# Kernel optimization log

Measured on AMD Instinct MI355X. Metric: run time of the kernel, lower is better.

## Reference

```python
import jax, jax.numpy as jnp
import numpy as np

B, QT, KT = 4, 1024, 1024
Q_SIZE, K_SIZE, EMB, HEADS = 1024, 1024, 1024, 8
HEAD_DIM = EMB // HEADS


def setup_inputs() -> dict:
    key = jax.random.key(0)
    ks = jax.random.split(key, 8)
    query = jax.random.normal(ks[0], (B, QT, Q_SIZE), dtype=jnp.float32)
    key_t = jax.random.normal(ks[1], (B, KT, K_SIZE), dtype=jnp.float32)
    mask = jax.random.randint(ks[2], (B, QT, KT), 0, 2, dtype=jnp.int32)
    # Linear weights stored as (in, out); torch Linear computes x @ W.T, equivalent here.
    sq = 1.0 / np.sqrt(Q_SIZE)
    sk = 1.0 / np.sqrt(K_SIZE)
    se = 1.0 / np.sqrt(EMB)
    Wq = jax.random.uniform(ks[3], (Q_SIZE, EMB), jnp.float32, -sq, sq)
    Wk = jax.random.uniform(ks[4], (K_SIZE, EMB), jnp.float32, -sk, sk)
    Wv = jax.random.uniform(ks[5], (K_SIZE, EMB), jnp.float32, -sk, sk)
    Wu = jax.random.uniform(ks[6], (EMB, EMB), jnp.float32, -se, se)
    bu = jax.random.uniform(ks[7], (EMB,), jnp.float32, -se, se)
    return {"query": query, "key": key_t, "mask": mask,
            "Wq": Wq, "Wk": Wk, "Wv": Wv, "Wu": Wu, "bu": bu}


def reference(query, key, mask, Wq, Wk, Wv, Wu, bu):
    b, q_t, _ = query.shape
    k_t = key.shape[1]
    q = (query @ Wq).reshape(b, q_t, HEADS, HEAD_DIM)   # b i n d
    k = (key @ Wk).reshape(b, k_t, HEADS, HEAD_DIM)     # b j n d
    v = (key @ Wv).reshape(b, k_t, HEADS, HEAD_DIM)
    # NOTE: original module defines self.scale but never applies it.
    att_score = jnp.einsum('bind,bjnd->bijn', q, k)
    att_score = jnp.where(mask[..., None] == 0, jnp.float32(-1e9), att_score)
    att_prob = jax.nn.softmax(att_score, axis=2)        # softmax over key axis j
    att_vec = jnp.einsum('bijn,bjnd->bind', att_prob, v).reshape(b, q_t, EMB)
    return att_vec @ Wu + bu
```

## Files before the change

### kernel.cpp

```cpp
#include <hip/hip_runtime.h>
#include <hip/hip_bf16.h>


typedef __attribute__((ext_vector_type(8))) short bf16x8;
typedef __attribute__((ext_vector_type(4))) float f32x4;

static constexpr int BB = 4;
static constexpr int TT = 1024;
static constexpr int EE = 1024;
static constexpr int HH = 8;
static constexpr int DD = 128;

static __device__ __forceinline__ unsigned short f2b(float x) {
  union { float f; unsigned int u; } c; c.f = x;
  unsigned int r = c.u + 0x7fffu + ((c.u >> 16) & 1u);
  return (unsigned short)(r >> 16);
}

static __device__ __forceinline__ unsigned int cvtpk(float lo, float hi) {
  unsigned int r;
  asm("v_cvt_pk_bf16_f32 %0, %1, %2" : "=v"(r) : "v"(lo), "v"(hi));
  return r;
}

static __device__ __forceinline__ float exp2x(float x) {
  float r;
  asm("v_exp_f32 %0, %1" : "=v"(r) : "v"(x));
  return r;
}

static __device__ __forceinline__ void gload_lds16(const void* g, void* l) {
  __builtin_amdgcn_global_load_lds(
      (const __attribute__((address_space(1))) unsigned int*)g,
      (__attribute__((address_space(3))) unsigned int*)l, 16, 0, 0);
}

__global__ __launch_bounds__(256) void cvt_kernel(
    const float* __restrict__ qf, const float* __restrict__ kf,
    unsigned short* __restrict__ qb, unsigned short* __restrict__ kb) {
  int i = blockIdx.x * 256 + threadIdx.x;
  float4 a = ((const float4*)qf)[i];
  ushort4 oa; oa.x = f2b(a.x); oa.y = f2b(a.y); oa.z = f2b(a.z); oa.w = f2b(a.w);
  ((ushort4*)qb)[i] = oa;
  float4 b = ((const float4*)kf)[i];
  ushort4 ob; ob.x = f2b(b.x); ob.y = f2b(b.y); ob.z = f2b(b.z); ob.w = f2b(b.w);
  ((ushort4*)kb)[i] = ob;
}

struct WT4 { const float* src[4]; unsigned short* dst[4]; float scale[4]; };

__global__ __launch_bounds__(256) void wtrans_kernel(WT4 wt) {
  const float* src = wt.src[blockIdx.z];
  unsigned short* dst = wt.dst[blockIdx.z];
  const float sc = wt.scale[blockIdx.z];
  __shared__ float tile[32][33];
  int n0 = blockIdx.x * 32, k0 = blockIdx.y * 32;
  int tx = threadIdx.x, ty = threadIdx.y;
#pragma unroll
  for (int i = 0; i < 4; ++i)
    tile[ty + i * 8][tx] = src[(size_t)(k0 + ty + i * 8) * EE + n0 + tx];
  __syncthreads();
#pragma unroll
  for (int i = 0; i < 4; ++i)
    dst[(size_t)(n0 + ty + i * 8) * EE + k0 + tx] = f2b(tile[tx][ty + i * 8] * sc);
}

__global__ __launch_bounds__(256) void vtrans_kernel(
    const unsigned short* __restrict__ vp, unsigned short* __restrict__ vt) {
  int bh = blockIdx.z; int b = bh >> 3, h = bh & 7;
  int d0 = blockIdx.x * 32, kt0 = blockIdx.y * 32;
  __shared__ unsigned short tile[32][33];
  int tx = threadIdx.x, ty = threadIdx.y;
#pragma unroll
  for (int i = 0; i < 4; ++i)
    tile[ty + i * 8][tx] =
        vp[(size_t)(b * TT + kt0 + ty + i * 8) * EE + h * DD + d0 + tx];
  __syncthreads();
#pragma unroll
  for (int i = 0; i < 4; ++i)
    vt[(size_t)((b * HH + h) * DD + d0 + ty + i * 8) * TT + kt0 + tx] =
        tile[tx][ty + i * 8];
}

__global__ __launch_bounds__(256) void maskpack_kernel(
    const int* __restrict__ mask, unsigned long long* __restrict__ mbits) {
  int row = blockIdx.x * 4 + (threadIdx.x >> 6);
  int lane = threadIdx.x & 63;
  const int* mrow = mask + (size_t)row * TT;
  unsigned long long myw = 0;
#pragma unroll
  for (int jw = 0; jw < 16; ++jw) {
    unsigned long long bal = __ballot(mrow[jw * 64 + lane] != 0);
    if (lane == jw) myw = bal;
  }
  if (lane < 16) mbits[(size_t)row * 16 + lane] = myw;
}

static __device__ __forceinline__ void gemm_core(
    const unsigned short* __restrict__ A, const unsigned short* __restrict__ Bt,
    unsigned short* __restrict__ Cb) {
  constexpr int K = EE, N = EE;
  __shared__ __align__(16) unsigned short As[128 * 64];
  __shared__ __align__(16) unsigned short Bs[128 * 64];
  const int tid = threadIdx.x, lane = tid & 63, w = tid >> 6;
  const int wm = w >> 1, wn = w & 1;
  const int bm = blockIdx.x, bn = blockIdx.y;
  const int g4 = lane >> 4, l15 = lane & 15;

  f32x4 acc[4][4] = {};

  for (int kt = 0; kt < K / 64; ++kt) {
    const int k0 = kt * 64;
#pragma unroll
    for (int it = 0; it < 4; ++it) {
      int idx = it * 256 + tid;
      int r = idx >> 3, c = (idx & 7) ^ (r & 7);
      gload_lds16(A + (size_t)(bm * 128 + r) * K + k0 + c * 8, As + idx * 8);
      gload_lds16(Bt + (size_t)(bn * 128 + r) * K + k0 + c * 8, Bs + idx * 8);
    }
    __syncthreads();
    bf16x8 af[2][4], bf[2][4];
#pragma unroll
    for (int kc2 = 0; kc2 < 2; ++kc2) {
      int co = ((kc2 * 4 + g4) ^ (l15 & 7)) * 8;
#pragma unroll
      for (int i = 0; i < 4; ++i) {
        af[kc2][i] = *(const bf16x8*)(As + (wm * 64 + i * 16 + l15) * 64 + co);
        bf[kc2][i] = *(const bf16x8*)(Bs + (wn * 64 + i * 16 + l15) * 64 + co);
      }
    }
#pragma unroll
    for (int kc2 = 0; kc2 < 2; ++kc2)
#pragma unroll
      for (int i = 0; i < 4; ++i)
#pragma unroll
        for (int j = 0; j < 4; ++j)
          acc[i][j] = __builtin_amdgcn_mfma_f32_16x16x32_bf16(
              af[kc2][i], bf[kc2][j], acc[i][j], 0, 0, 0);
    __syncthreads();
  }

  const int rr = g4 * 4;
#pragma unroll
  for (int i = 0; i < 4; ++i)
#pragma unroll
    for (int j = 0; j < 4; ++j) {
      int row = bm * 128 + wm * 64 + i * 16 + rr;
      int col = bn * 128 + wn * 64 + j * 16 + l15;
#pragma unroll
      for (int r = 0; r < 4; ++r)
        Cb[(size_t)(row + r) * N + col] = f2b(acc[i][j][r]);
    }
}

struct Gemm3 { const unsigned short* A[3]; const unsigned short* Bt[3];
               unsigned short* C[3]; };

__global__ __launch_bounds__(256) void proj_gemm_kernel(Gemm3 g) {
  int z = blockIdx.z;
  gemm_core(g.A[z], g.Bt[z], g.C[z]);
}

__global__ __launch_bounds__(256) void out_gemm_kernel(
    const unsigned short* __restrict__ A, const unsigned short* __restrict__ Bt,
    float* __restrict__ Cf, const float* __restrict__ bias) {
  constexpr int K = EE, N = EE;
  __shared__ __align__(16) unsigned short As[64 * 32];
  __shared__ __align__(16) unsigned short Bs[128 * 32];
  const int tid = threadIdx.x, lane = tid & 63, w = tid >> 6;
  const int wm = w >> 1, wn = w & 1;
  const int bm = blockIdx.x, bn = blockIdx.y;
  const int g4 = lane >> 4, l15 = lane & 15;

  f32x4 acc[2][4] = {};

  for (int kt = 0; kt < K / 32; ++kt) {
    const int k0 = kt * 32;
    {
      int row = tid >> 2, c = tid & 3;
      gload_lds16(A + (size_t)(bm * 64 + row) * K + k0 + c * 8, As + tid * 8);
    }
#pragma unroll
    for (int it = 0; it < 2; ++it) {
      int idx = it * 256 + tid;
      int row = idx >> 2, c = idx & 3;
      gload_lds16(Bt + (size_t)(bn * 128 + row) * K + k0 + c * 8, Bs + idx * 8);
    }
    __syncthreads();
    bf16x8 af[2], bf[4];
#pragma unroll
    for (int i = 0; i < 2; ++i)
      af[i] = *(const bf16x8*)(As + (wm * 32 + i * 16 + l15) * 32 + g4 * 8);
#pragma unroll
    for (int j = 0; j < 4; ++j)
      bf[j] = *(const bf16x8*)(Bs + (wn * 64 + j * 16 + l15) * 32 + g4 * 8);
#pragma unroll
    for (int i = 0; i < 2; ++i)
#pragma unroll
      for (int j = 0; j < 4; ++j)
        acc[i][j] = __builtin_amdgcn_mfma_f32_16x16x32_bf16(af[i], bf[j],
                                                            acc[i][j], 0, 0, 0);
    __syncthreads();
  }

  const int rr = g4 * 4;
#pragma unroll
  for (int i = 0; i < 2; ++i)
#pragma unroll
    for (int j = 0; j < 4; ++j) {
      int row = bm * 64 + wm * 32 + i * 16 + rr;
      int col = bn * 128 + wn * 64 + j * 16 + l15;
#pragma unroll
      for (int r = 0; r < 4; ++r)
        Cf[(size_t)(row + r) * N + col] = acc[i][j][r] + bias[col];
    }
}

__global__ __launch_bounds__(256) void attn_kernel(
    const unsigned short* __restrict__ q, const unsigned short* __restrict__ k,
    const unsigned short* __restrict__ vt,
    const unsigned long long* __restrict__ mbits,
    unsigned short* __restrict__ av) {
  extern __shared__ __align__(16) char smem[];

  const int tid = threadIdx.x, lane = tid & 63, w = tid >> 6;
  const int orig = blockIdx.x + 16 * blockIdx.y + 128 * blockIdx.z;
  const int qt = (orig >> 3) & 15;
  const int pair = ((orig & 7) << 2) | (orig >> 7);
  const int h = pair & 7, b = pair >> 3;
  const int i0 = qt * 64 + w * 16;
  const int g4 = lane >> 4, l15 = lane & 15;
  const int swz = (l15 & 7) << 4;

  bf16x8 aq[4];
  {
    const unsigned short* qb =
        q + (size_t)(b * TT + i0 + l15) * EE + h * DD + g4 * 8;
#pragma unroll
    for (int kc = 0; kc < 4; ++kc) aq[kc] = *(const bf16x8*)(qb + kc * 32);
  }

  const unsigned short* kb0 = k + (size_t)(b * TT) * EE + h * DD;
  const unsigned short* vb0 = vt + (size_t)((b * HH + h) * DD) * TT;
  const unsigned short* kptr[4];
  const unsigned short* vptr[4];
  int chunkb[4];
#pragma unroll
  for (int p = 0; p < 4; ++p) {
    int base = p * 256 + w * 64;
    int idx = base + lane;
    int kr = idx >> 4, kcc = (idx & 15) ^ (kr & 7);
    kptr[p] = kb0 + (size_t)kr * EE + kcc * 8;
    int vr = idx >> 3, vcc = (idx & 7) ^ (vr & 7);
    vptr[p] = vb0 + (size_t)vr * TT + vcc * 8;
    chunkb[p] = base * 16;
  }

  const unsigned long long* mb = mbits + ((size_t)(b * TT + i0 + l15) << 4);
  unsigned long long mcur = mb[0];

  int kb_[4], vb_[2];
#pragma unroll
  for (int kc = 0; kc < 4; ++kc)
    kb_[kc] = l15 * 256 + ((kc * 64 + g4 * 16) ^ swz);
#pragma unroll
  for (int h2 = 0; h2 < 2; ++h2)
    vb_[h2] = 32768 + l15 * 128 + ((h2 * 64 + g4 * 16) ^ swz);

#pragma unroll
  for (int p = 0; p < 4; ++p) {
    gload_lds16(kptr[p], smem + chunkb[p]);
    gload_lds16(vptr[p], smem + 32768 + chunkb[p]);
  }
#pragma unroll
  for (int p = 0; p < 4; ++p) { kptr[p] += 64 * EE; vptr[p] += 64; }

  f32x4 oacc[8] = {};
  float mrun = -__builtin_inff(), lrun = 0.f;

  __syncthreads();
  int bufoff = 0;

  for (int t = 0; t < 16; ++t) {
    if (t > 0) __builtin_amdgcn_s_barrier();

    unsigned long long mnext = 0;
    if (t < 15) {
      mnext = mb[t + 1];
      int dst = bufoff ^ 16384;
#pragma unroll
      for (int p = 0; p < 4; ++p) {
        gload_lds16(kptr[p], smem + dst + chunkb[p]);
        gload_lds16(vptr[p], smem + 32768 + dst + chunkb[p]);
      }
#pragma unroll
      for (int p = 0; p < 4; ++p) { kptr[p] += 64 * EE; vptr[p] += 64; }
      asm volatile("s_waitcnt vmcnt(8)" ::: "memory");
      __builtin_amdgcn_sched_barrier(0);
    } else {
      asm volatile("s_waitcnt vmcnt(0)" ::: "memory");
      __builtin_amdgcn_sched_barrier(0);
    }

    f32x4 sacc[4] = {};
    __builtin_amdgcn_s_setprio(1);
#pragma unroll
    for (int kc = 0; kc < 4; ++kc)
#pragma unroll
      for (int nt = 0; nt < 4; ++nt) {
        bf16x8 bk = *(const bf16x8*)(smem + kb_[kc] + nt * 4096);
        sacc[nt] = __builtin_amdgcn_mfma_f32_16x16x32_bf16(bk, aq[kc],
                                                           sacc[nt], 0, 0, 0);
      }
    __builtin_amdgcn_s_setprio(0);

    {
      unsigned int wlo = (unsigned int)mcur, whi = (unsigned int)(mcur >> 32);
#pragma unroll
      for (int nt = 0; nt < 4; ++nt) {
        unsigned int ww = (nt < 2) ? wlo : whi;
        int bb = (nt & 1) * 16 + g4 * 4;
#pragma unroll
        for (int r = 0; r < 4; ++r)
          if (((ww >> (bb + r)) & 1u) == 0u) sacc[nt][r] = -1e9f;
      }
    }

    float mx = sacc[0][0];
#pragma unroll
    for (int nt = 0; nt < 4; ++nt)
#pragma unroll
      for (int r = 0; r < 4; ++r) mx = fmaxf(mx, sacc[nt][r]);
    mx = fmaxf(mx, __shfl_xor(mx, 16, 64));
    mx = fmaxf(mx, __shfl_xor(mx, 32, 64));

    if (__any(mx > mrun + 8.f)) {
      float mnew = fmaxf(mrun, mx);
      float sc = exp2x(mrun - mnew);
      lrun *= sc;
      mrun = mnew;
      float scO[4];
#pragma unroll
      for (int r = 0; r < 4; ++r)
        scO[r] = __shfl(sc, (lane & 48) | (((lane & 48) >> 2) + r), 64);
#pragma unroll
      for (int dt = 0; dt < 8; ++dt)
#pragma unroll
        for (int r = 0; r < 4; ++r) oacc[dt][r] *= scO[r];
    }

    float p[4][4];
    float s0 = 0.f;
#pragma unroll
    for (int nt = 0; nt < 4; ++nt)
#pragma unroll
      for (int r = 0; r < 4; ++r) {
        float pv = exp2x(sacc[nt][r] - mrun);
        p[nt][r] = pv;
        s0 += pv;
      }
    s0 += __shfl_xor(s0, 16, 64);
    s0 += __shfl_xor(s0, 32, 64);
    lrun += s0;

    unsigned int paw[2][4];
#pragma unroll
    for (int h2 = 0; h2 < 2; ++h2) {
      unsigned int D0a = cvtpk(p[2 * h2][0], p[2 * h2][1]);
      unsigned int D1a = cvtpk(p[2 * h2][2], p[2 * h2][3]);
      unsigned int D0b = cvtpk(p[2 * h2 + 1][0], p[2 * h2 + 1][1]);
      unsigned int D1b = cvtpk(p[2 * h2 + 1][2], p[2 * h2 + 1][3]);
      unsigned int r1 = __shfl_xor(g4 < 2 ? D0a : D0b, 16, 64);
      unsigned int r2 = __shfl_xor(g4 < 2 ? D1a : D1b, 16, 64);
      unsigned int r3 = __shfl_xor(g4 == 0 ? D0b : D0a, 32, 64);
      unsigned int r4 = __shfl_xor(g4 == 0 ? D1b : D1a, 32, 64);
      unsigned int r5 = __shfl_xor(g4 == 2 ? D0a : D0b, 48, 64);
      unsigned int r6 = __shfl_xor(g4 == 2 ? D1a : D1b, 48, 64);
      paw[h2][0] = g4 == 0 ? D0a : g4 == 1 ? r5 : g4 == 2 ? r3 : r1;
      paw[h2][1] = g4 == 0 ? D1a : g4 == 1 ? r6 : g4 == 2 ? r4 : r2;
      paw[h2][2] = g4 == 0 ? r1 : g4 == 1 ? r3 : g4 == 2 ? r5 : D0b;
      paw[h2][3] = g4 == 0 ? r2 : g4 == 1 ? r4 : g4 == 2 ? r6 : D1b;
    }

    __builtin_amdgcn_s_setprio(1);
#pragma unroll
    for (int h2 = 0; h2 < 2; ++h2) {
      union { unsigned int u[4]; bf16x8 v; } pau;
      pau.u[0] = paw[h2][0]; pau.u[1] = paw[h2][1];
      pau.u[2] = paw[h2][2]; pau.u[3] = paw[h2][3];
#pragma unroll
      for (int dt = 0; dt < 8; ++dt) {
        bf16x8 bv = *(const bf16x8*)(smem + vb_[h2] + dt * 2048);
        oacc[dt] = __builtin_amdgcn_mfma_f32_16x16x32_bf16(pau.v, bv, oacc[dt],
                                                           0, 0, 0);
      }
    }
    __builtin_amdgcn_s_setprio(0);

    bufoff ^= 16384;
#pragma unroll
    for (int kc = 0; kc < 4; ++kc) kb_[kc] ^= 16384;
#pragma unroll
    for (int h2 = 0; h2 < 2; ++h2) vb_[h2] ^= 16384;
    mcur = mnext;
  }

  float linv[4];
#pragma unroll
  for (int r = 0; r < 4; ++r)
    linv[r] = 1.f / __shfl(lrun, (lane & 48) | (((lane & 48) >> 2) + r), 64);
  unsigned short* ob =
      av + (size_t)(b * TT + i0 + g4 * 4) * EE + h * DD + l15;
#pragma unroll
  for (int dt = 0; dt < 8; ++dt)
#pragma unroll
    for (int r = 0; r < 4; ++r)
      ob[(size_t)r * EE + dt * 16] = f2b(oacc[dt][r] * linv[r]);
}

extern "C" void kernel_launch(void* const* d_in, const int* in_sizes, int n_in,
                              void* d_out, int out_size, void* d_ws,
                              size_t ws_size, hipStream_t stream) {
  const float* query = (const float*)d_in[0];
  const float* key   = (const float*)d_in[1];
  const int*   mask  = (const int*)d_in[2];
  const float* Wq    = (const float*)d_in[3];
  const float* Wk    = (const float*)d_in[4];
  const float* Wv    = (const float*)d_in[5];
  const float* Wu    = (const float*)d_in[6];
  const float* bu    = (const float*)d_in[7];
  float* out = (float*)d_out;

  char* ws = (char*)d_ws;
  const size_t MB = 1024 * 1024;
  unsigned short* qbf = (unsigned short*)(ws);
  unsigned short* kbf = (unsigned short*)(ws + 8 * MB);
  unsigned short* Wqt = (unsigned short*)(ws + 16 * MB);
  unsigned short* Wkt = (unsigned short*)(ws + 18 * MB);
  unsigned short* Wvt = (unsigned short*)(ws + 20 * MB);
  unsigned short* Wut = (unsigned short*)(ws + 22 * MB);
  unsigned short* qp  = (unsigned short*)(ws + 24 * MB);
  unsigned short* kp  = (unsigned short*)(ws + 32 * MB);
  unsigned short* vp  = (unsigned short*)(ws + 40 * MB);
  unsigned short* vtb = (unsigned short*)(ws + 48 * MB);
  unsigned short* av  = (unsigned short*)(ws + 56 * MB);
  unsigned long long* mbt = (unsigned long long*)(ws + 40 * MB);

  cvt_kernel<<<4096, 256, 0, stream>>>(query, key, qbf, kbf);

  WT4 wt; wt.src[0] = Wq; wt.src[1] = Wk; wt.src[2] = Wv; wt.src[3] = Wu;
  wt.dst[0] = Wqt; wt.dst[1] = Wkt; wt.dst[2] = Wvt; wt.dst[3] = Wut;
  wt.scale[0] = 1.4426950408889634f;
  wt.scale[1] = 1.0f; wt.scale[2] = 1.0f; wt.scale[3] = 1.0f;
  wtrans_kernel<<<dim3(32, 32, 4), dim3(32, 8), 0, stream>>>(wt);

  Gemm3 g3;
  g3.A[0] = qbf; g3.A[1] = kbf; g3.A[2] = kbf;
  g3.Bt[0] = Wqt; g3.Bt[1] = Wkt; g3.Bt[2] = Wvt;
  g3.C[0] = qp; g3.C[1] = kp; g3.C[2] = vp;
  proj_gemm_kernel<<<dim3(32, 8, 3), 256, 0, stream>>>(g3);

  vtrans_kernel<<<dim3(4, 32, 32), dim3(32, 8), 0, stream>>>(vp, vtb);

  maskpack_kernel<<<1024, 256, 0, stream>>>(mask, mbt);

  attn_kernel<<<dim3(16, 8, 4), 256, 65536, stream>>>(qp, kp, vtb, mbt, av);

  out_gemm_kernel<<<dim3(64, 8), 256, 0, stream>>>(av, Wut, out, bu);
}
```

Baseline: 118.0 us.

## Split attention key range across two wave groups with flash-decoding style merge

Doubles the attention block to 512 threads: two groups of four waves each process half of every key tile (32 keys) for the same 64 query rows, keeping separate running max/sum and output accumulators. At the end one group writes its partial output and statistics to shared memory and the other merges them with rescaling before writing bf16 results. Loads are reorganised so K is loaded by four waves and V by the other four, and the explicit vmcnt waits are replaced by a trailing __syncthreads. The aim is more waves per block to hide latency, at the cost of extra merge work, LDS traffic and looser memory-wait ordering.

```diff
diff --git a/kernel.cpp b/kernel.cpp
--- a/kernel.cpp
+++ b/kernel.cpp
@@ -216,7 +216,7 @@
     }
 }
 
-__global__ __launch_bounds__(256) void attn_kernel(
+__global__ __launch_bounds__(512, 4) void attn_kernel(
     const unsigned short* __restrict__ q, const unsigned short* __restrict__ k,
     const unsigned short* __restrict__ vt,
     const unsigned long long* __restrict__ mbits,
@@ -224,11 +224,12 @@
   extern __shared__ __align__(16) char smem[];
 
   const int tid = threadIdx.x, lane = tid & 63, w = tid >> 6;
+  const int grp = w >> 2, qw = w & 3;
   const int orig = blockIdx.x + 16 * blockIdx.y + 128 * blockIdx.z;
   const int qt = (orig >> 3) & 15;
   const int pair = ((orig & 7) << 2) | (orig >> 7);
   const int h = pair & 7, b = pair >> 3;
-  const int i0 = qt * 64 + w * 16;
+  const int i0 = qt * 64 + qw * 16;
   const int g4 = lane >> 4, l15 = lane & 15;
   const int swz = (l15 & 7) << 4;
 
@@ -240,40 +241,47 @@
     for (int kc = 0; kc < 4; ++kc) aq[kc] = *(const bf16x8*)(qb + kc * 32);
   }
 
-  const unsigned short* kb0 = k + (size_t)(b * TT) * EE + h * DD;
-  const unsigned short* vb0 = vt + (size_t)((b * HH + h) * DD) * TT;
-  const unsigned short* kptr[4];
-  const unsigned short* vptr[4];
-  int chunkb[4];
-#pragma unroll
-  for (int p = 0; p < 4; ++p) {
-    int base = p * 256 + w * 64;
-    int idx = base + lane;
-    int kr = idx >> 4, kcc = (idx & 15) ^ (kr & 7);
-    kptr[p] = kb0 + (size_t)kr * EE + kcc * 8;
-    int vr = idx >> 3, vcc = (idx & 7) ^ (vr & 7);
-    vptr[p] = vb0 + (size_t)vr * TT + vcc * 8;
-    chunkb[p] = base * 16;
-  }
-
-  const unsigned long long* mb = mbits + ((size_t)(b * TT + i0 + l15) << 4);
-  unsigned long long mcur = mb[0];
-
-  int kb_[4], vb_[2];
+  const unsigned short* sptr[4];
+  int ldsb[4];
+  size_t sadv;
+  if (w < 4) {
+    int kg = w >> 1, kh = w & 1;
+    const unsigned short* kb0 = k + (size_t)(b * TT) * EE + h * DD;
+#pragma unroll
+    for (int p = 0; p < 4; ++p) {
+      int idx = kh * 256 + p * 64 + lane;
+      int kr = idx >> 4, c = (idx & 15) ^ (kr & 7);
+      sptr[p] = kb0 + (size_t)(kg * 512 + kr) * EE + c * 8;
+      ldsb[p] = kg * 8192 + (kh * 256 + p * 64) * 16;
+    }
+    sadv = (size_t)32 * EE;
+  } else {
+    int vw = w - 4;
+    const unsigned short* vb0 = vt + (size_t)((b * HH + h) * DD) * TT;
+#pragma unroll
+    for (int p = 0; p < 4; ++p) {
+      int cid = vw * 256 + p * 64 + lane;
+      int d = cid >> 3, slot = cid & 7, eff = slot ^ (d & 7);
+      sptr[p] = vb0 + (size_t)d * TT + (eff >> 2) * 512 + (eff & 3) * 8;
+      ldsb[p] = 32768 + (vw * 256 + p * 64) * 16;
+    }
+    sadv = 32;
+  }
+
+  const unsigned* mb32 =
+      (const unsigned*)mbits + ((size_t)(b * TT + i0 + l15) << 5) + grp * 16;
+  unsigned mcur = mb32[0];
+
+  int kb_[4];
 #pragma unroll
   for (int kc = 0; kc < 4; ++kc)
-    kb_[kc] = l15 * 256 + ((kc * 64 + g4 * 16) ^ swz);
-#pragma unroll
-  for (int h2 = 0; h2 < 2; ++h2)
-    vb_[h2] = 32768 + l15 * 128 + ((h2 * 64 + g4 * 16) ^ swz);
-
-#pragma unroll
-  for (int p = 0; p < 4; ++p) {
-    gload_lds16(kptr[p], smem + chunkb[p]);
-    gload_lds16(vptr[p], smem + 32768 + chunkb[p]);
-  }
-#pragma unroll
-  for (int p = 0; p < 4; ++p) { kptr[p] += 64 * EE; vptr[p] += 64; }
+    kb_[kc] = grp * 8192 + l15 * 256 + ((kc * 64 + g4 * 16) ^ swz);
+  const int vb_ = 32768 + l15 * 128 + (((grp * 4 + g4) ^ (l15 & 7)) << 4);
+
+#pragma unroll
+  for (int p = 0; p < 4; ++p) gload_lds16(sptr[p], smem + ldsb[p]);
+#pragma unroll
+  for (int p = 0; p < 4; ++p) sptr[p] += sadv;
 
   f32x4 oacc[8] = {};
   float mrun = -__builtin_inff(), lrun = 0.f;
@@ -282,53 +290,38 @@
   int bufoff = 0;
 
   for (int t = 0; t < 16; ++t) {
-    if (t > 0) __builtin_amdgcn_s_barrier();
-
-    unsigned long long mnext = 0;
+    unsigned mnext = 0;
     if (t < 15) {
-      mnext = mb[t + 1];
+      mnext = mb32[t + 1];
       int dst = bufoff ^ 16384;
 #pragma unroll
-      for (int p = 0; p < 4; ++p) {
-        gload_lds16(kptr[p], smem + dst + chunkb[p]);
-        gload_lds16(vptr[p], smem + 32768 + dst + chunkb[p]);
-      }
-#pragma unroll
-      for (int p = 0; p < 4; ++p) { kptr[p] += 64 * EE; vptr[p] += 64; }
-      asm volatile("s_waitcnt vmcnt(8)" ::: "memory");
-      __builtin_amdgcn_sched_barrier(0);
-    } else {
-      asm volatile("s_waitcnt vmcnt(0)" ::: "memory");
-      __builtin_amdgcn_sched_barrier(0);
-    }
-
-    f32x4 sacc[4] = {};
+      for (int p = 0; p < 4; ++p) gload_lds16(sptr[p], smem + dst + ldsb[p]);
+#pragma unroll
+      for (int p = 0; p < 4; ++p) sptr[p] += sadv;
+    }
+
+    f32x4 sacc[2] = {};
     __builtin_amdgcn_s_setprio(1);
 #pragma unroll
     for (int kc = 0; kc < 4; ++kc)
 #pragma unroll
-      for (int nt = 0; nt < 4; ++nt) {
-        bf16x8 bk = *(const bf16x8*)(smem + kb_[kc] + nt * 4096);
+      for (int nt = 0; nt < 2; ++nt) {
+        bf16x8 bk = *(const bf16x8*)(smem + bufoff + kb_[kc] + nt * 4096);
         sacc[nt] = __builtin_amdgcn_mfma_f32_16x16x32_bf16(bk, aq[kc],
                                                            sacc[nt], 0, 0, 0);
       }
     __builtin_amdgcn_s_setprio(0);
 
-    {
-      unsigned int wlo = (unsigned int)mcur, whi = (unsigned int)(mcur >> 32);
-#pragma unroll
-      for (int nt = 0; nt < 4; ++nt) {
-        unsigned int ww = (nt < 2) ? wlo : whi;
-        int bb = (nt & 1) * 16 + g4 * 4;
-#pragma unroll
-        for (int r = 0; r < 4; ++r)
-          if (((ww >> (bb + r)) & 1u) == 0u) sacc[nt][r] = -1e9f;
-      }
-    }
+#pragma unroll
+    for (int nt = 0; nt < 2; ++nt)
+#pragma unroll
+      for (int r = 0; r < 4; ++r)
+        if (((mcur >> (nt * 16 + g4 * 4 + r)) & 1u) == 0u)
+          sacc[nt][r] = -1e9f;
 
     float mx = sacc[0][0];
 #pragma unroll
-    for (int nt = 0; nt < 4; ++nt)
+    for (int nt = 0; nt < 2; ++nt)
 #pragma unroll
       for (int r = 0; r < 4; ++r) mx = fmaxf(mx, sacc[nt][r]);
     mx = fmaxf(mx, __shfl_xor(mx, 16, 64));
@@ -349,73 +342,92 @@
         for (int r = 0; r < 4; ++r) oacc[dt][r] *= scO[r];
     }
 
-    float p[4][4];
+    float p2[2][4];
     float s0 = 0.f;
 #pragma unroll
-    for (int nt = 0; nt < 4; ++nt)
+    for (int nt = 0; nt < 2; ++nt)
 #pragma unroll
       for (int r = 0; r < 4; ++r) {
         float pv = exp2x(sacc[nt][r] - mrun);
-        p[nt][r] = pv;
+        p2[nt][r] = pv;
         s0 += pv;
       }
     s0 += __shfl_xor(s0, 16, 64);
     s0 += __shfl_xor(s0, 32, 64);
     lrun += s0;
 
-    unsigned int paw[2][4];
-#pragma unroll
-    for (int h2 = 0; h2 < 2; ++h2) {
-      unsigned int D0a = cvtpk(p[2 * h2][0], p[2 * h2][1]);
-      unsigned int D1a = cvtpk(p[2 * h2][2], p[2 * h2][3]);
-      unsigned int D0b = cvtpk(p[2 * h2 + 1][0], p[2 * h2 + 1][1]);
-      unsigned int D1b = cvtpk(p[2 * h2 + 1][2], p[2 * h2 + 1][3]);
+    unsigned int paw[4];
+    {
+      unsigned int D0a = cvtpk(p2[0][0], p2[0][1]);
+      unsigned int D1a = cvtpk(p2[0][2], p2[0][3]);
+      unsigned int D0b = cvtpk(p2[1][0], p2[1][1]);
+      unsigned int D1b = cvtpk(p2[1][2], p2[1][3]);
       unsigned int r1 = __shfl_xor(g4 < 2 ? D0a : D0b, 16, 64);
       unsigned int r2 = __shfl_xor(g4 < 2 ? D1a : D1b, 16, 64);
       unsigned int r3 = __shfl_xor(g4 == 0 ? D0b : D0a, 32, 64);
       unsigned int r4 = __shfl_xor(g4 == 0 ? D1b : D1a, 32, 64);
       unsigned int r5 = __shfl_xor(g4 == 2 ? D0a : D0b, 48, 64);
       unsigned int r6 = __shfl_xor(g4 == 2 ? D1a : D1b, 48, 64);
-      paw[h2][0] = g4 == 0 ? D0a : g4 == 1 ? r5 : g4 == 2 ? r3 : r1;
-      paw[h2][1] = g4 == 0 ? D1a : g4 == 1 ? r6 : g4 == 2 ? r4 : r2;
-      paw[h2][2] = g4 == 0 ? r1 : g4 == 1 ? r3 : g4 == 2 ? r5 : D0b;
-      paw[h2][3] = g4 == 0 ? r2 : g4 == 1 ? r4 : g4 == 2 ? r6 : D1b;
+      paw[0] = g4 == 0 ? D0a : g4 == 1 ? r5 : g4 == 2 ? r3 : r1;
+      paw[1] = g4 == 0 ? D1a : g4 == 1 ? r6 : g4 == 2 ? r4 : r2;
+      paw[2] = g4 == 0 ? r1 : g4 == 1 ? r3 : g4 == 2 ? r5 : D0b;
+      paw[3] = g4 == 0 ? r2 : g4 == 1 ? r4 : g4 == 2 ? r6 : D1b;
     }
 
     __builtin_amdgcn_s_setprio(1);
-#pragma unroll
-    for (int h2 = 0; h2 < 2; ++h2) {
+    {
       union { unsigned int u[4]; bf16x8 v; } pau;
-      pau.u[0] = paw[h2][0]; pau.u[1] = paw[h2][1];
-      pau.u[2] = paw[h2][2]; pau.u[3] = paw[h2][3];
+      pau.u[0] = paw[0]; pau.u[1] = paw[1];
+      pau.u[2] = paw[2]; pau.u[3] = paw[3];
 #pragma unroll
       for (int dt = 0; dt < 8; ++dt) {
-        bf16x8 bv = *(const bf16x8*)(smem + vb_[h2] + dt * 2048);
+        bf16x8 bv = *(const bf16x8*)(smem + bufoff + vb_ + dt * 2048);
         oacc[dt] = __builtin_amdgcn_mfma_f32_16x16x32_bf16(pau.v, bv, oacc[dt],
                                                            0, 0, 0);
       }
     }
     __builtin_amdgcn_s_setprio(0);
 
+    __syncthreads();
     bufoff ^= 16384;
-#pragma unroll
-    for (int kc = 0; kc < 4; ++kc) kb_[kc] ^= 16384;
-#pragma unroll
-    for (int h2 = 0; h2 < 2; ++h2) vb_[h2] ^= 16384;
     mcur = mnext;
   }
 
-  float linv[4];
-#pragma unroll
-  for (int r = 0; r < 4; ++r)
-    linv[r] = 1.f / __shfl(lrun, (lane & 48) | (((lane & 48) >> 2) + r), 64);
-  unsigned short* ob =
-      av + (size_t)(b * TT + i0 + g4 * 4) * EE + h * DD + l15;
-#pragma unroll
-  for (int dt = 0; dt < 8; ++dt)
-#pragma unroll
-    for (int r = 0; r < 4; ++r)
-      ob[(size_t)r * EE + dt * 16] = f2b(oacc[dt][r] * linv[r]);
+  if (grp == 1) {
+    char* ob = smem + qw * 8192 + lane * 128;
+#pragma unroll
+    for (int dt = 0; dt < 8; ++dt)
+      *(f32x4*)(ob + ((dt ^ (lane & 7)) * 16)) = oacc[dt];
+    float* mlb = (float*)(smem + 32768 + qw * 512 + lane * 8);
+    mlb[0] = mrun; mlb[1] = lrun;
+  }
+  __syncthreads();
+  if (grp == 0) {
+    const char* ob = smem + qw * 8192 + lane * 128;
+    const float* mlb = (const float*)(smem + 32768 + qw * 512 + lane * 8);
+    float m2 = mlb[0], l2 = mlb[1];
+    float ms = fmaxf(mrun, m2);
+    float a1 = exp2x(mrun - ms), a2 = exp2x(m2 - ms);
+    float lt = lrun * a1 + l2 * a2;
+    float a1O[4], a2O[4], linv[4];
+#pragma unroll
+    for (int r = 0; r < 4; ++r) {
+      int src = (lane & 48) | (((lane & 48) >> 2) + r);
+      a1O[r] = __shfl(a1, src, 64);
+      a2O[r] = __shfl(a2, src, 64);
+      linv[r] = 1.f / __shfl(lt, src, 64);
+    }
+    unsigned short* obp =
+        av + (size_t)(b * TT + i0 + g4 * 4) * EE + h * DD + l15;
+#pragma unroll
+    for (int dt = 0; dt < 8; ++dt) {
+      f32x4 o2 = *(const f32x4*)(ob + ((dt ^ (lane & 7)) * 16));
+#pragma unroll
+      for (int r = 0; r < 4; ++r)
+        obp[(size_t)r * EE + dt * 16] =
+            f2b((oacc[dt][r] * a1O[r] + o2[r] * a2O[r]) * linv[r]);
+    }
+  }
 }
 
 extern "C" void kernel_launch(void* const* d_in, const int* in_sizes, int n_in,
@@ -464,7 +476,7 @@
 
   maskpack_kernel<<<1024, 256, 0, stream>>>(mask, mbt);
 
-  attn_kernel<<<dim3(16, 8, 4), 256, 65536, stream>>>(qp, kp, vtb, mbt, av);
+  attn_kernel<<<dim3(16, 8, 4), 512, 65536, stream>>>(qp, kp, vtb, mbt, av);
 
   out_gemm_kernel<<<dim3(64, 8), 256, 0, stream>>>(av, Wut, out, bu);
 }
```

Result: faster. 115.1 us (-2.5%).
